# Kernel tuning notes

Hardware: AMD Instinct MI355X
Metric: run time of the kernel (lower is better)

The kernel has to match this reference:

```python
import jax, jax.numpy as jnp
import numpy as np
import math

DEPTH = 2
RATIOS = (0.5, 0.5)
K_PROP = 2  # Gra_inc(2)


def _prop(x, ei, ew, K=K_PROP):
    # GCN-style sym-normalized diffusion with implicit self-loops; Gra_inc(K)
    N = x.shape[0]
    row, col = ei[0], ei[1]
    deg = jax.ops.segment_sum(ew, row, num_segments=N) + 1.0  # +1 self-loop
    dinv = jax.lax.rsqrt(deg)
    norm = dinv[row] * ew * dinv[col]          # [E]
    self_n = (dinv * dinv)[:, None]            # [N,1]
    h, out = x, x
    for _ in range(K):
        h = jax.ops.segment_sum(norm[:, None] * h[col], row, num_segments=N) + self_n * h
        out = out + h
    return out


def _conv(x, ei, ew, W):
    return _prop(x @ W, ei, ew)


def _pool(x, ei, ew, pw, ratio):
    # PyG TopKPooling: score = tanh(x.pw/||pw||), keep top ceil(ratio*N) nodes,
    # gate features by score, relabel surviving edges (dropped edges -> weight 0).
    N = x.shape[0]
    k = int(math.ceil(ratio * N))
    score = jnp.tanh(x @ pw / jnp.linalg.norm(pw))
    val, perm = jax.lax.top_k(score, k)
    x2 = x[perm] * val[:, None]
    nm = jnp.full((N,), -1, jnp.int32).at[perm].set(jnp.arange(k, dtype=jnp.int32))
    r, c = nm[ei[0]], nm[ei[1]]
    kept = (r >= 0) & (c >= 0)
    ei2 = jnp.stack([jnp.where(kept, r, 0), jnp.where(kept, c, 0)])
    ew2 = jnp.where(kept, ew, 0.0)
    return x2, ei2, ew2, perm


def setup_inputs() -> dict:
    key = jax.random.key(0)
    ks = jax.random.split(key, 10)
    N, E, C_in, C_hid, C_out = 50000, 800000, 128, 128, 64
    def w(k, i, o):
        return jax.random.normal(k, (i, o), jnp.float32) / np.sqrt(i)
    return {
        "x": jax.random.normal(ks[0], (N, C_in), jnp.float32),
        "edge_index": jax.random.randint(ks[1], (2, E), 0, N, dtype=jnp.int32),
        "Wd0": w(ks[2], C_in, C_hid),
        "Wd1": w(ks[3], C_hid, C_hid),
        "Wd2": w(ks[4], C_hid, C_hid),
        "pw0": jax.random.normal(ks[5], (C_hid,), jnp.float32) / np.sqrt(C_hid),
        "pw1": jax.random.normal(ks[6], (C_hid,), jnp.float32) / np.sqrt(C_hid),
        "Wu0": w(ks[7], C_hid, C_hid),
        "Wu1": w(ks[8], C_hid, C_hid),
        "Wu2": w(ks[9], 2 * C_hid, C_out),
    }


def reference(x, edge_index, Wd0, Wd1, Wd2, pw0, pw1, Wu0, Wu1, Wu2):
    ei = edge_index
    ew = jnp.ones((ei.shape[1],), x.dtype)
    x = jax.nn.relu(_conv(x, ei, ew, Wd0))
    org = x
    xs, eis, ews, perms = [x], [ei], [ew], []
    for i, (pw, Wd) in enumerate(zip((pw0, pw1), (Wd1, Wd2))):
        x, ei, ew, perm = _pool(x, ei, ew, pw, RATIOS[i])
        x = jax.nn.relu(_conv(x, ei, ew, Wd))
        if i < DEPTH - 1:
            xs.append(x); eis.append(ei); ews.append(ew)
        perms.append(perm)
    for i, Wu in enumerate((Wu0, Wu1)):
        j = DEPTH - 1 - i
        res, ei, ew, perm = xs[j], eis[j], ews[j], perms[j]
        up = jnp.zeros_like(res).at[perm].set(x)
        x = res + up  # sum_res skip fusion
        x = _conv(x, ei, ew, Wu)
        if i < DEPTH - 1:
            x = jax.nn.relu(x)
    x = jnp.concatenate([x, org], axis=1)
    return _conv(x, ei, ew, Wu2)
```

## Files before the change

kernel.cpp:

```cpp
#include <hip/hip_runtime.h>
#include <hip/hip_bf16.h>
#include <stdint.h>

#define DEV __device__ __forceinline__

static constexpr int C_HID = 128;

DEV float4 f4_fma(float a, float4 w, float4 acc) {
  acc.x = fmaf(a, w.x, acc.x); acc.y = fmaf(a, w.y, acc.y);
  acc.z = fmaf(a, w.z, acc.z); acc.w = fmaf(a, w.w, acc.w);
  return acc;
}

DEV unsigned bfpack2(float a, float b) {
  unsigned ua = __float_as_uint(a), ub = __float_as_uint(b);
  ua += 0x7FFF + ((ua >> 16) & 1);
  ub += 0x7FFF + ((ub >> 16) & 1);
  return (ua >> 16) | (ub & 0xFFFF0000u);
}
DEV uint2 bfpack4(float4 v) { return make_uint2(bfpack2(v.x, v.y), bfpack2(v.z, v.w)); }
DEV float4 bfunpack4(uint2 u) {
  return make_float4(__uint_as_float(u.x << 16), __uint_as_float(u.x & 0xFFFF0000u),
                     __uint_as_float(u.y << 16), __uint_as_float(u.y & 0xFFFF0000u));
}

__global__ void scorekeys_kernel(const float* __restrict__ x, const float* __restrict__ pw,
                                 float* __restrict__ score, unsigned long long* __restrict__ keys,
                                 int N) {
  int row = blockIdx.x * 4 + (threadIdx.x >> 6);
  int lane = threadIdx.x & 63;
  if (row >= N) return;
  float p0 = pw[lane], p1 = pw[lane + 64];
  float pn = p0 * p0 + p1 * p1;
  const float* xr = x + (size_t)row * C_HID;
  float s = xr[lane] * p0 + xr[lane + 64] * p1;
#pragma unroll
  for (int o = 32; o > 0; o >>= 1) {
    s += __shfl_xor(s, o, 64);
    pn += __shfl_xor(pn, o, 64);
  }
  if (lane == 0) {
    float sc = tanhf(s / sqrtf(pn));
    score[row] = sc;
    unsigned u = __float_as_uint(sc);
    u ^= (u >> 31) ? 0xFFFFFFFFu : 0x80000000u;
    keys[row] = (((unsigned long long)(~u)) << 16) | (unsigned)row;
  }
}

__global__ void select_hist1_kernel(const unsigned long long* __restrict__ keys, int N,
                                    int* __restrict__ hist) {
  int i = blockIdx.x * 256 + threadIdx.x;
  if (i >= N) return;
  int bin = (int)((keys[i] >> 32) & 0xFFFF);
  atomicAdd(&hist[bin + ((blockIdx.x & 3) << 16)], 1);
}

__global__ void hist_merge_kernel(int* __restrict__ hist) {
  int b = blockIdx.x * 256 + threadIdx.x;
  hist[b] = hist[b] + hist[b + 65536] + hist[b + 2 * 65536] + hist[b + 3 * 65536];
}

__global__ void select_hist_kernel(const unsigned long long* __restrict__ keys, int N,
                                   const unsigned long long* __restrict__ prefix,
                                   int shift, unsigned long long M, int* __restrict__ hist) {
  int i = blockIdx.x * 256 + threadIdx.x;
  if (i >= N) return;
  unsigned long long P = *prefix;
  unsigned long long key = keys[i];
  if (((key ^ P) & M) == 0)
    atomicAdd(&hist[(int)((key >> shift) & 0xFFFF)], 1);
}

__global__ void select_find_kernel(const int* __restrict__ hist,
                                   unsigned long long* __restrict__ prefix,
                                   int* __restrict__ rem, int shift, int* __restrict__ ctr,
                                   int k) {
  int t = threadIdx.x;
  int base = t * 64;
  int s = 0;
#pragma unroll
  for (int j = 0; j < 64; ++j) s += hist[base + j];
  int lane = t & 63, w = t >> 6;
  int v = s;
  for (int o = 1; o < 64; o <<= 1) { int u = __shfl_up(v, o, 64); if (lane >= o) v += u; }
  __shared__ int ws[16];
  if (lane == 63) ws[w] = v;
  __syncthreads();
  if (t < 16) {
    int u = ws[t];
    for (int o = 1; o < 16; o <<= 1) { int uu = __shfl_up(u, o, 64); if (t >= o) u += uu; }
    ws[t] = u;
  }
  __syncthreads();
  int incl = v + (w > 0 ? ws[w - 1] : 0);
  int excl = incl - s;
  int R = (shift == 32) ? k : *rem;
  if (excl < R && incl >= R) {
    int c = excl, b = base;
    for (int j = 0; j < 64; ++j) {
      int h = hist[base + j];
      if (c + h >= R) { b = base + j; break; }
      c += h;
    }
    if (shift == 32) *prefix = ((unsigned long long)b) << shift;
    else             *prefix |= ((unsigned long long)b) << shift;
    *rem = R - c;
    if (shift == 0) *ctr = 0;
  }
}

__global__ void select_enum_kernel(const unsigned long long* __restrict__ keys, int N,
                                   const unsigned long long* __restrict__ Tptr,
                                   int* __restrict__ ctr, int* __restrict__ perm,
                                   int* __restrict__ nm) {
  int i = blockIdx.x * 256 + threadIdx.x;
  if (i >= N) return;
  unsigned long long T = *Tptr;
  if (keys[i] <= T) { int r = atomicAdd(ctr, 1); perm[r] = i; nm[i] = r; }
  else nm[i] = -1;
}

__global__ void pool_gather_kernel(const float* __restrict__ xold, const float* __restrict__ score,
                                   const int* __restrict__ perm, float* __restrict__ xnew, int k) {
  int j = blockIdx.x * 2 + (threadIdx.x >> 7);
  int f = threadIdx.x & 127;
  if (j >= k) return;
  int src = perm[j];
  xnew[(size_t)j * C_HID + f] = xold[(size_t)src * C_HID + f] * score[src];
}

DEV bool map_edge(int a, int b, const int* m0, const int* m1, int& r, int& c) {
  r = a; c = b;
  if (m0) { r = m0[r]; c = m0[c]; if ((r | c) < 0) return false; }
  if (m1) { r = m1[r]; c = m1[c]; if ((r | c) < 0) return false; }
  return true;
}

__global__ void edge_count_kernel(const int* __restrict__ ei, int E, int* __restrict__ cnt) {
  int e = blockIdx.x * 256 + threadIdx.x;
  if (e >= E) return;
  atomicAdd(&cnt[ei[e]], 1);
}

__global__ void edge_fill_kernel(const int* __restrict__ ei, int E,
                                 const int* __restrict__ rowptr, int* __restrict__ fc,
                                 int* __restrict__ colv) {
  int e = blockIdx.x * 256 + threadIdx.x;
  if (e >= E) return;
  int r = ei[e], c = ei[E + e];
  int pos = rowptr[r] + atomicAdd(&fc[r], 1);
  colv[pos] = c;
}

#define CEPT 7
__global__ __launch_bounds__(1024) void edge_count_compact_kernel(
    const int* __restrict__ ei, int E, const int* m0, const int* m1,
    int* __restrict__ cnt, int2* __restrict__ pairs, int* __restrict__ pctr) {
  int tid = threadIdx.x;
  int gbase = blockIdx.x * (1024 * CEPT) + tid;
  int rs[CEPT], cs[CEPT];
  int myn = 0;
#pragma unroll
  for (int i = 0; i < CEPT; ++i) {
    int e = gbase + i * 1024;
    int r, c;
    bool keep = (e < E) && map_edge(ei[e], ei[E + e], m0, m1, r, c);
    rs[i] = keep ? r : -1;
    cs[i] = keep ? c : 0;
    if (keep) { atomicAdd(&cnt[r], 1); ++myn; }
  }
  int lane = tid & 63, w = tid >> 6;
  int v = myn;
  for (int o = 1; o < 64; o <<= 1) { int u = __shfl_up(v, o, 64); if (lane >= o) v += u; }
  __shared__ int ws[16];
  __shared__ int bbase;
  if (lane == 63) ws[w] = v;
  __syncthreads();
  if (tid < 16) {
    int u = ws[tid];
    for (int o = 1; o < 16; o <<= 1) { int uu = __shfl_up(u, o, 64); if (tid >= o) u += uu; }
    ws[tid] = u;
  }
  __syncthreads();
  int excl = v - myn + (w > 0 ? ws[w - 1] : 0);
  if (tid == 1023) bbase = atomicAdd(pctr, excl + myn);
  __syncthreads();
  int pos = bbase + excl;
#pragma unroll
  for (int i = 0; i < CEPT; ++i)
    if (rs[i] >= 0) pairs[pos++] = make_int2(rs[i], cs[i]);
}

__global__ void edge_fill_compact_kernel(const int2* __restrict__ pairs, const int* __restrict__ pctr,
                                         const int* __restrict__ rowptr, int* __restrict__ fc,
                                         int* __restrict__ colv) {
  int i = blockIdx.x * 256 + threadIdx.x;
  if (i >= *pctr) return;
  int2 pr = pairs[i];
  int pos = rowptr[pr.x] + atomicAdd(&fc[pr.x], 1);
  colv[pos] = pr.y;
}

__global__ void scan_partial_kernel(const int* __restrict__ cnt, int n, int* __restrict__ bsum) {
  int i = blockIdx.x * 256 + threadIdx.x;
  int v = (i < n) ? cnt[i] : 0;
#pragma unroll
  for (int o = 32; o > 0; o >>= 1) v += __shfl_down(v, o, 64);
  __shared__ int ws[4];
  if ((threadIdx.x & 63) == 0) ws[threadIdx.x >> 6] = v;
  __syncthreads();
  if (threadIdx.x == 0) bsum[blockIdx.x] = ws[0] + ws[1] + ws[2] + ws[3];
}

__global__ void scan_blocksums_kernel(int* __restrict__ bsum, int nb) {
  int t = threadIdx.x;
  int v = (t < nb) ? bsum[t] : 0;
  int lane = t & 63, w = t >> 6;
  for (int o = 1; o < 64; o <<= 1) { int u = __shfl_up(v, o, 64); if (lane >= o) v += u; }
  __shared__ int ws[16];
  if (lane == 63) ws[w] = v;
  __syncthreads();
  if (t < 16) {
    int u = ws[t];
    for (int o = 1; o < 16; o <<= 1) { int uu = __shfl_up(u, o, 64); if (t >= o) u += uu; }
    ws[t] = u;
  }
  __syncthreads();
  if (t < nb) bsum[t] = v + (w > 0 ? ws[w - 1] : 0);
}

__global__ void scan_scatter_kernel(const int* __restrict__ cnt, int n,
                                    const int* __restrict__ bsum,
                                    int* __restrict__ rowptr, float* __restrict__ dinv,
                                    int* __restrict__ fc) {
  int i = blockIdx.x * 256 + threadIdx.x;
  int v = (i < n) ? cnt[i] : 0;
  int lane = threadIdx.x & 63, w = threadIdx.x >> 6;
  int s = v;
  for (int o = 1; o < 64; o <<= 1) { int u = __shfl_up(s, o, 64); if (lane >= o) s += u; }
  __shared__ int ws[4];
  __shared__ int wo[4];
  if (lane == 63) ws[w] = s;
  __syncthreads();
  if (threadIdx.x == 0) { int c = 0; for (int j = 0; j < 4; ++j) { wo[j] = c; c += ws[j]; } }
  __syncthreads();
  int excl = s - v + wo[w] + (blockIdx.x > 0 ? bsum[blockIdx.x - 1] : 0);
  if (i < n) {
    rowptr[i] = excl;
    dinv[i] = rsqrtf((float)v + 1.0f);
    fc[i] = 0;
    if (i == n - 1) rowptr[n] = excl + v;
  }
}

template <int FIRST, int RELU>
__global__ void spmm_kernel(const int* __restrict__ rowptr, const int* __restrict__ colv,
                            const float* __restrict__ dinv,
                            const float* __restrict__ h_in, const float* __restrict__ x0,
                            float* __restrict__ out, int M, int C) {
  int lanes = C >> 2;
  int rpb = 256 / lanes;
  int r = blockIdx.x * rpb + (int)threadIdx.x / lanes;
  int lane = (int)threadIdx.x % lanes;
  if (r >= M) return;
  float d = dinv[r];
  const float4* hin4 = (const float4*)h_in;
  size_t base = (size_t)r * lanes + lane;
  float4 self = hin4[base];
  float sn = d * d;
  float4 v = make_float4(sn * self.x, sn * self.y, sn * self.z, sn * self.w);
  int e0 = rowptr[r], e1 = rowptr[r + 1];
  int e = e0;
  for (; e + 8 <= e1; e += 8) {
    int cc[8];
#pragma unroll
    for (int i = 0; i < 8; ++i) cc[i] = colv[e + i];
    float4 hh[8];
#pragma unroll
    for (int i = 0; i < 8; ++i) hh[i] = hin4[(size_t)cc[i] * lanes + lane];
    float ww[8];
#pragma unroll
    for (int i = 0; i < 8; ++i) ww[i] = d * dinv[cc[i]];
#pragma unroll
    for (int i = 0; i < 8; ++i) v = f4_fma(ww[i], hh[i], v);
  }
  for (; e < e1; ++e) {
    int c = colv[e];
    float w = d * dinv[c];
    float4 h = hin4[(size_t)c * lanes + lane];
    v = f4_fma(w, h, v);
  }
  if (FIRST) {
    ((float4*)out)[base] = v;
  } else {
    float4 a = ((const float4*)x0)[base];
    a.x += self.x + v.x; a.y += self.y + v.y; a.z += self.z + v.z; a.w += self.w + v.w;
    if (RELU) { a.x = fmaxf(a.x, 0.f); a.y = fmaxf(a.y, 0.f); a.z = fmaxf(a.z, 0.f); a.w = fmaxf(a.w, 0.f); }
    ((float4*)out)[base] = a;
  }
}

template <int FIRST, int RELU>
__global__ void spmm_bf16_kernel(const int* __restrict__ rowptr, const int* __restrict__ colv,
                                 const float* __restrict__ dinv,
                                 const ushort* __restrict__ hb, const float* __restrict__ x0,
                                 void* __restrict__ outp, int M, int C) {
  int lanes = C >> 2;
  int rpb = 256 / lanes;
  int r = blockIdx.x * rpb + (int)threadIdx.x / lanes;
  int lane = (int)threadIdx.x % lanes;
  if (r >= M) return;
  float d = dinv[r];
  const uint2* hb2 = (const uint2*)hb;
  size_t base = (size_t)r * lanes + lane;
  float4 self = bfunpack4(hb2[base]);
  float sn = d * d;
  float4 v = make_float4(sn * self.x, sn * self.y, sn * self.z, sn * self.w);
  int e0 = rowptr[r], e1 = rowptr[r + 1];
  int e = e0;
  for (; e + 8 <= e1; e += 8) {
    int cc[8];
#pragma unroll
    for (int i = 0; i < 8; ++i) cc[i] = colv[e + i];
    uint2 hh[8];
#pragma unroll
    for (int i = 0; i < 8; ++i) hh[i] = hb2[(size_t)cc[i] * lanes + lane];
    float ww[8];
#pragma unroll
    for (int i = 0; i < 8; ++i) ww[i] = d * dinv[cc[i]];
#pragma unroll
    for (int i = 0; i < 8; ++i) v = f4_fma(ww[i], bfunpack4(hh[i]), v);
  }
  for (; e < e1; ++e) {
    int c = colv[e];
    float w = d * dinv[c];
    v = f4_fma(w, bfunpack4(hb2[(size_t)c * lanes + lane]), v);
  }
  if (FIRST) {
    ((uint2*)outp)[base] = bfpack4(v);
  } else {
    float4 a = ((const float4*)x0)[base];
    a.x += self.x + v.x; a.y += self.y + v.y; a.z += self.z + v.z; a.w += self.w + v.w;
    if (RELU) { a.x = fmaxf(a.x, 0.f); a.y = fmaxf(a.y, 0.f); a.z = fmaxf(a.z, 0.f); a.w = fmaxf(a.w, 0.f); }
    ((float4*)outp)[base] = a;
  }
}

template <int NC, int KT, int SKIP, int ADDIN, int MIRROR>
__global__ __launch_bounds__(256) void gemm_kernel(const float* __restrict__ A1, int K1,
                                                   const float* __restrict__ W,
                                                   float* __restrict__ Cd, int M,
                                                   const float* __restrict__ up,
                                                   const int* __restrict__ nm,
                                                   const float* __restrict__ addv,
                                                   ushort* __restrict__ bh) {
  constexpr int KTILE = 32;
  constexpr int AP = KTILE + 4;
  constexpr int CG = NC / 4;
  constexpr int RG = 256 / CG;
  constexpr int RPT = 64 / RG;
  __shared__ float Wl[KTILE * NC];
  __shared__ float Al[64 * AP];
  int tid = threadIdx.x;
  int r0 = blockIdx.x * 64;
  int cg = tid % CG, rg = tid / CG;
  float4 acc[RPT];
#pragma unroll
  for (int m = 0; m < RPT; ++m) acc[m] = make_float4(0.f, 0.f, 0.f, 0.f);

  for (int k0 = 0; k0 < KT; k0 += KTILE) {
    const float4* Wg = (const float4*)(W + (size_t)k0 * NC);
    for (int idx = tid; idx < KTILE * NC / 4; idx += 256)
      ((float4*)Wl)[idx] = Wg[idx];
#pragma unroll
    for (int s = 0; s < (64 * KTILE / 4) / 256; ++s) {
      int f4i = tid + s * 256;
      int row = f4i >> 3;
      int kk = (f4i & 7) << 2;
      int gr = r0 + row, gk = k0 + kk;
      float4 v = make_float4(0.f, 0.f, 0.f, 0.f);
      if (gr < M) {
        v = *(const float4*)(A1 + (size_t)gr * K1 + gk);
        if (SKIP) {
          int j = nm[gr];
          if (j >= 0) {
            float4 u = *(const float4*)(up + (size_t)j * K1 + gk);
            v.x += u.x; v.y += u.y; v.z += u.z; v.w += u.w;
          }
        }
      }
      *(float4*)&Al[row * AP + kk] = v;
    }
    __syncthreads();
#pragma unroll
    for (int kk0 = 0; kk0 < KTILE; kk0 += 4) {
      float4 a4[RPT];
#pragma unroll
      for (int m = 0; m < RPT; ++m)
        a4[m] = *(const float4*)&Al[(rg * RPT + m) * AP + kk0];
#pragma unroll
      for (int j = 0; j < 4; ++j) {
        float4 w = *(const float4*)&Wl[(kk0 + j) * NC + cg * 4];
#pragma unroll
        for (int m = 0; m < RPT; ++m) {
          float a = (j == 0) ? a4[m].x : (j == 1) ? a4[m].y : (j == 2) ? a4[m].z : a4[m].w;
          acc[m] = f4_fma(a, w, acc[m]);
        }
      }
    }
    __syncthreads();
  }
#pragma unroll
  for (int m = 0; m < RPT; ++m) {
    int gr = r0 + rg * RPT + m;
    if (gr < M) {
      float4 o = acc[m];
      if (ADDIN) {
        float4 u = *(const float4*)(addv + (size_t)gr * NC + cg * 4);
        o.x += u.x; o.y += u.y; o.z += u.z; o.w += u.w;
      }
      *(float4*)(Cd + (size_t)gr * NC + cg * 4) = o;
      if (MIRROR) ((uint2*)bh)[(size_t)gr * CG + cg] = bfpack4(o);
    }
  }
}

extern "C" void kernel_launch(void* const* d_in, const int* in_sizes, int n_in,
                              void* d_out, int out_size, void* d_ws, size_t ws_size,
                              hipStream_t stream) {
  const float* x   = (const float*)d_in[0];
  const int*   ei  = (const int*)d_in[1];
  const float* Wd0 = (const float*)d_in[2];
  const float* Wd1 = (const float*)d_in[3];
  const float* Wd2 = (const float*)d_in[4];
  const float* pw0 = (const float*)d_in[5];
  const float* pw1 = (const float*)d_in[6];
  const float* Wu0 = (const float*)d_in[7];
  const float* Wu1 = (const float*)d_in[8];
  const float* Wu2 = (const float*)d_in[9];
  float* out = (float*)d_out;

  const int C = C_HID;
  int N0 = in_sizes[0] / C;
  int E  = in_sizes[1] / 2;
  int k1 = (N0 + 1) / 2;
  int k2 = (k1 + 1) / 2;

  char* p = (char*)d_ws;
  auto alloc = [&](size_t bytes) { char* q = p; p += (bytes + 255) & ~(size_t)255; return q; };
  float* org   = (float*)alloc((size_t)N0 * C * 4);
  float* b0    = (float*)alloc((size_t)N0 * C * 4);
  float* b1    = (float*)alloc((size_t)N0 * C * 4);
  float* b2    = (float*)alloc((size_t)N0 * C * 4);
  float* x1res = (float*)alloc((size_t)k1 * C * 4);
  ushort* bh   = (ushort*)alloc((size_t)N0 * C * 2);
  ushort* h1h  = (ushort*)alloc((size_t)N0 * C * 2);
  float* score = (float*)alloc((size_t)N0 * 4);
  unsigned long long* keys = (unsigned long long*)alloc((size_t)N0 * 8);
  int* perm0 = (int*)alloc((size_t)k1 * 4);
  int* perm1 = (int*)alloc((size_t)k2 * 4);
  int* map0  = (int*)alloc((size_t)N0 * 4);
  int* map1  = (int*)alloc((size_t)k1 * 4);
  int* cnt   = (int*)alloc((size_t)N0 * 4);
  int* fc    = (int*)alloc((size_t)N0 * 4);
  int* rp0   = (int*)alloc((size_t)(N0 + 1) * 4);
  int* rp1   = (int*)alloc((size_t)(k1 + 1) * 4);
  int* rp2   = (int*)alloc((size_t)(k2 + 1) * 4);
  float* dinv0 = (float*)alloc((size_t)N0 * 4);
  float* dinv1 = (float*)alloc((size_t)k1 * 4);
  float* dinv2 = (float*)alloc((size_t)k2 * 4);
  int* col0 = (int*)alloc((size_t)E * 4);
  int* col1 = (int*)alloc((size_t)E * 4);
  int* col2 = (int*)alloc((size_t)E * 4);
  int2* pairs = (int2*)alloc((size_t)E * 8);
  int* hist12 = (int*)alloc((size_t)12 * 65536 * 4);
  int* bsum = (int*)alloc(1024 * 4);
  float* Wcat1 = (float*)alloc((size_t)128 * 64 * 4);
  unsigned long long* selT = (unsigned long long*)alloc(64);
  int* selRem = (int*)alloc(64);
  int* selCtr = (int*)alloc(64);
  int* pctr = (int*)alloc(64);

  dim3 b256(256);
  int egrid = (E + 255) / 256;
  int cgrid = (E + 1024 * CEPT - 1) / (1024 * CEPT);
  int g0_128 = (N0 + 7) / 8;
  int g1_128 = (k1 + 7) / 8;
  int g2_128 = (k2 + 7) / 8;
  int g0_64  = (N0 + 15) / 16;

  auto scan_csr = [&](int n, int* rowptr, float* dinv) {
    int g = (n + 255) / 256;
    scan_partial_kernel<<<g, b256, 0, stream>>>(cnt, n, bsum);
    scan_blocksums_kernel<<<1, 1024, 0, stream>>>(bsum, g);
    scan_scatter_kernel<<<g, b256, 0, stream>>>(cnt, n, bsum, rowptr, dinv, fc);
  };

  auto topk_select = [&](int N, int k, int* perm, int* nm, int* histb) {
    int g = (N + 255) / 256;
    select_hist1_kernel<<<g, b256, 0, stream>>>(keys, N, histb);
    hist_merge_kernel<<<256, b256, 0, stream>>>(histb);
    select_find_kernel<<<1, 1024, 0, stream>>>(histb, selT, selRem, 32, selCtr, k);
    select_hist_kernel<<<g, b256, 0, stream>>>(keys, N, selT, 16, ~0ull << 32, histb + 4 * 65536);
    select_find_kernel<<<1, 1024, 0, stream>>>(histb + 4 * 65536, selT, selRem, 16, selCtr, k);
    select_hist_kernel<<<g, b256, 0, stream>>>(keys, N, selT, 0, ~0ull << 16, histb + 5 * 65536);
    select_find_kernel<<<1, 1024, 0, stream>>>(histb + 5 * 65536, selT, selRem, 0, selCtr, k);
    select_enum_kernel<<<g, b256, 0, stream>>>(keys, N, selT, selCtr, perm, nm);
  };

  hipMemsetAsync(hist12, 0, (size_t)12 * 65536 * 4, stream);

  gemm_kernel<64, 128, 0, 0, 0><<<2, b256, 0, stream>>>(Wu1, 128, Wu2, Wcat1, 128, nullptr, nullptr, nullptr, nullptr);

  hipMemsetAsync(cnt, 0, (size_t)N0 * 4, stream);
  edge_count_kernel<<<egrid, b256, 0, stream>>>(ei, E, cnt);
  scan_csr(N0, rp0, dinv0);
  edge_fill_kernel<<<egrid, b256, 0, stream>>>(ei, E, rp0, fc, col0);

  gemm_kernel<128, 128, 0, 0, 0><<<(N0 + 63) / 64, b256, 0, stream>>>(x, 128, Wd0, b0, N0, nullptr, nullptr, nullptr, nullptr);
  spmm_kernel<1, 0><<<g0_128, b256, 0, stream>>>(rp0, col0, dinv0, b0, nullptr, b1, N0, 128);
  spmm_kernel<0, 1><<<g0_128, b256, 0, stream>>>(rp0, col0, dinv0, b1, b0, org, N0, 128);

  scorekeys_kernel<<<(N0 + 3) / 4, b256, 0, stream>>>(org, pw0, score, keys, N0);
  topk_select(N0, k1, perm0, map0, hist12);
  pool_gather_kernel<<<(k1 + 1) / 2, b256, 0, stream>>>(org, score, perm0, b0, k1);

  hipMemsetAsync(cnt, 0, (size_t)k1 * 4, stream);
  hipMemsetAsync(pctr, 0, 4, stream);
  edge_count_compact_kernel<<<cgrid, 1024, 0, stream>>>(ei, E, map0, nullptr, cnt, pairs, pctr);
  scan_csr(k1, rp1, dinv1);
  edge_fill_compact_kernel<<<egrid, b256, 0, stream>>>(pairs, pctr, rp1, fc, col1);

  gemm_kernel<128, 128, 0, 0, 0><<<(k1 + 63) / 64, b256, 0, stream>>>(b0, 128, Wd1, b1, k1, nullptr, nullptr, nullptr, nullptr);
  spmm_kernel<1, 0><<<g1_128, b256, 0, stream>>>(rp1, col1, dinv1, b1, nullptr, b2, k1, 128);
  spmm_kernel<0, 1><<<g1_128, b256, 0, stream>>>(rp1, col1, dinv1, b2, b1, x1res, k1, 128);

  scorekeys_kernel<<<(k1 + 3) / 4, b256, 0, stream>>>(x1res, pw1, score, keys, k1);
  topk_select(k1, k2, perm1, map1, hist12 + 6 * 65536);
  pool_gather_kernel<<<(k2 + 1) / 2, b256, 0, stream>>>(x1res, score, perm1, b0, k2);

  hipMemsetAsync(cnt, 0, (size_t)k2 * 4, stream);
  hipMemsetAsync(pctr, 0, 4, stream);
  edge_count_compact_kernel<<<cgrid, 1024, 0, stream>>>(ei, E, map0, map1, cnt, pairs, pctr);
  scan_csr(k2, rp2, dinv2);
  edge_fill_compact_kernel<<<egrid, b256, 0, stream>>>(pairs, pctr, rp2, fc, col2);

  gemm_kernel<128, 128, 0, 0, 1><<<(k2 + 63) / 64, b256, 0, stream>>>(b0, 128, Wd2, b1, k2, nullptr, nullptr, nullptr, bh);
  spmm_bf16_kernel<1, 0><<<g2_128, b256, 0, stream>>>(rp2, col2, dinv2, bh, nullptr, h1h, k2, 128);
  spmm_bf16_kernel<0, 1><<<g2_128, b256, 0, stream>>>(rp2, col2, dinv2, h1h, b1, b0, k2, 128);

  gemm_kernel<128, 128, 1, 0, 1><<<(k1 + 63) / 64, b256, 0, stream>>>(x1res, 128, Wu0, b1, k1, b0, map1, nullptr, bh);
  spmm_bf16_kernel<1, 0><<<g1_128, b256, 0, stream>>>(rp1, col1, dinv1, bh, nullptr, h1h, k1, 128);
  spmm_bf16_kernel<0, 1><<<g1_128, b256, 0, stream>>>(rp1, col1, dinv1, h1h, b1, b0, k1, 128);

  gemm_kernel<64, 128, 1, 0, 1><<<(N0 + 63) / 64, b256, 0, stream>>>(org, 128, Wcat1, b2, N0, b0, map0, nullptr, bh);
  spmm_bf16_kernel<1, 0><<<g0_64, b256, 0, stream>>>(rp0, col0, dinv0, bh, nullptr, h1h, N0, 64);
  spmm_bf16_kernel<0, 0><<<g0_64, b256, 0, stream>>>(rp0, col0, dinv0, h1h, b2, b2, N0, 64);
  gemm_kernel<64, 128, 0, 1, 1><<<(N0 + 63) / 64, b256, 0, stream>>>(org, 128, Wu2 + (size_t)128 * 64, b0, N0, nullptr, nullptr, b2, bh);
  spmm_bf16_kernel<1, 0><<<g0_64, b256, 0, stream>>>(rp0, col0, dinv0, bh, nullptr, h1h, N0, 64);
  spmm_bf16_kernel<0, 0><<<g0_64, b256, 0, stream>>>(rp0, col0, dinv0, h1h, b0, out, N0, 64);
}
```

Measured before the change: 766.6 us.

## Fuse top-k selection and CSR build into persistent cooperative kernels

Replaces the chain of small top-k radix-select kernels and the count/scan/fill CSR kernels with two cooperative kernels that use grid-wide syncs between phases, removing many launches and memsets. The top-k find step now uses a two-level group sum read by one block, and enumeration uses block-level scan with one atomic per block. Grid syncs over 512 blocks add their own cost, and the grid-stride loops change parallelism and atomic contention compared with one-thread-per-element launches.

```diff
diff --git a/kernel.cpp b/kernel.cpp
--- a/kernel.cpp
+++ b/kernel.cpp
@@ -1,6 +1,9 @@
 #include <hip/hip_runtime.h>
 #include <hip/hip_bf16.h>
+#include <hip/hip_cooperative_groups.h>
 #include <stdint.h>
+
+namespace cg = cooperative_groups;
 
 #define DEV __device__ __forceinline__
 
@@ -48,77 +51,105 @@
   }
 }
 
-__global__ void select_hist1_kernel(const unsigned long long* __restrict__ keys, int N,
-                                    int* __restrict__ hist) {
-  int i = blockIdx.x * 256 + threadIdx.x;
-  if (i >= N) return;
-  int bin = (int)((keys[i] >> 32) & 0xFFFF);
-  atomicAdd(&hist[bin + ((blockIdx.x & 3) << 16)], 1);
-}
-
-__global__ void hist_merge_kernel(int* __restrict__ hist) {
-  int b = blockIdx.x * 256 + threadIdx.x;
-  hist[b] = hist[b] + hist[b + 65536] + hist[b + 2 * 65536] + hist[b + 3 * 65536];
-}
-
-__global__ void select_hist_kernel(const unsigned long long* __restrict__ keys, int N,
-                                   const unsigned long long* __restrict__ prefix,
-                                   int shift, unsigned long long M, int* __restrict__ hist) {
-  int i = blockIdx.x * 256 + threadIdx.x;
-  if (i >= N) return;
-  unsigned long long P = *prefix;
-  unsigned long long key = keys[i];
-  if (((key ^ P) & M) == 0)
-    atomicAdd(&hist[(int)((key >> shift) & 0xFFFF)], 1);
-}
-
-__global__ void select_find_kernel(const int* __restrict__ hist,
-                                   unsigned long long* __restrict__ prefix,
-                                   int* __restrict__ rem, int shift, int* __restrict__ ctr,
-                                   int k) {
-  int t = threadIdx.x;
-  int base = t * 64;
-  int s = 0;
-#pragma unroll
-  for (int j = 0; j < 64; ++j) s += hist[base + j];
-  int lane = t & 63, w = t >> 6;
-  int v = s;
-  for (int o = 1; o < 64; o <<= 1) { int u = __shfl_up(v, o, 64); if (lane >= o) v += u; }
-  __shared__ int ws[16];
-  if (lane == 63) ws[w] = v;
-  __syncthreads();
-  if (t < 16) {
-    int u = ws[t];
-    for (int o = 1; o < 16; o <<= 1) { int uu = __shfl_up(u, o, 64); if (t >= o) u += uu; }
-    ws[t] = u;
-  }
-  __syncthreads();
-  int incl = v + (w > 0 ? ws[w - 1] : 0);
-  int excl = incl - s;
-  int R = (shift == 32) ? k : *rem;
-  if (excl < R && incl >= R) {
-    int c = excl, b = base;
-    for (int j = 0; j < 64; ++j) {
-      int h = hist[base + j];
-      if (c + h >= R) { b = base + j; break; }
-      c += h;
-    }
-    if (shift == 32) *prefix = ((unsigned long long)b) << shift;
-    else             *prefix |= ((unsigned long long)b) << shift;
-    *rem = R - c;
-    if (shift == 0) *ctr = 0;
-  }
-}
-
-__global__ void select_enum_kernel(const unsigned long long* __restrict__ keys, int N,
-                                   const unsigned long long* __restrict__ Tptr,
-                                   int* __restrict__ ctr, int* __restrict__ perm,
-                                   int* __restrict__ nm) {
-  int i = blockIdx.x * 256 + threadIdx.x;
-  if (i >= N) return;
-  unsigned long long T = *Tptr;
-  if (keys[i] <= T) { int r = atomicAdd(ctr, 1); perm[r] = i; nm[i] = r; }
-  else nm[i] = -1;
+__global__ void topk_kernel(const unsigned long long* __restrict__ keys, int N, int k,
+                            int* __restrict__ hist, int* __restrict__ gsum,
+                            unsigned long long* __restrict__ prefixp, int* __restrict__ remp,
+                            int* __restrict__ ctr, int* __restrict__ perm,
+                            int* __restrict__ nm) {
+  cg::grid_group grid = cg::this_grid();
+  int gtid = blockIdx.x * blockDim.x + threadIdx.x;
+  int nthreads = gridDim.x * blockDim.x;
+
+  for (int i = gtid; i < 6 * 65536; i += nthreads) hist[i] = 0;
+  if (gtid == 0) *ctr = 0;
+  grid.sync();
+
+  for (int i = gtid; i < N; i += nthreads)
+    atomicAdd(&hist[(int)((keys[i] >> 32) & 0xFFFF) + ((blockIdx.x & 3) << 16)], 1);
+  grid.sync();
+  for (int b = gtid; b < 65536; b += nthreads)
+    hist[b] += hist[b + 65536] + hist[b + 2 * 65536] + hist[b + 3 * 65536];
+  grid.sync();
+
+  for (int pass = 0; pass < 3; ++pass) {
+    int shift = 32 - 16 * pass;
+    int* h = (pass == 0) ? hist : hist + (3 + pass) * 65536;
+    if (pass > 0) {
+      unsigned long long M = (pass == 1) ? (~0ull << 32) : (~0ull << 16);
+      unsigned long long P = *prefixp;
+      for (int i = gtid; i < N; i += nthreads) {
+        unsigned long long key = keys[i];
+        if (((key ^ P) & M) == 0)
+          atomicAdd(&h[(int)((key >> shift) & 0xFFFF)], 1);
+      }
+      grid.sync();
+    }
+    if (gtid < 1024) {
+      int s = 0, base = gtid * 64;
+      for (int j = 0; j < 64; ++j) s += h[base + j];
+      gsum[gtid] = s;
+    }
+    grid.sync();
+    if (blockIdx.x == 0) {
+      int t = threadIdx.x;
+      int s = gsum[4 * t] + gsum[4 * t + 1] + gsum[4 * t + 2] + gsum[4 * t + 3];
+      int lane = t & 63, w = t >> 6;
+      int v = s;
+      for (int o = 1; o < 64; o <<= 1) { int u = __shfl_up(v, o, 64); if (lane >= o) v += u; }
+      __shared__ int ws[4];
+      __shared__ int wo[4];
+      if (lane == 63) ws[w] = v;
+      __syncthreads();
+      if (t == 0) { int c = 0; for (int j = 0; j < 4; ++j) { wo[j] = c; c += ws[j]; } }
+      __syncthreads();
+      int incl = v + wo[w];
+      int excl = incl - s;
+      int R = (pass == 0) ? k : *remp;
+      if (excl < R && incl >= R) {
+        int c = excl, bfound = -1;
+        for (int g = 4 * t; g < 4 * t + 4 && bfound < 0; ++g) {
+          if (c + gsum[g] >= R) {
+            int base = g * 64;
+            for (int j = 0; j < 64; ++j) {
+              int hv = h[base + j];
+              if (c + hv >= R) { bfound = base + j; break; }
+              c += hv;
+            }
+          } else c += gsum[g];
+        }
+        if (pass == 0) *prefixp = ((unsigned long long)bfound) << shift;
+        else           *prefixp |= ((unsigned long long)bfound) << shift;
+        *remp = R - c;
+      }
+      __syncthreads();
+    }
+    grid.sync();
+  }
+
+  unsigned long long T = *prefixp;
+  for (int base = blockIdx.x * 256; base < N; base += nthreads) {
+    int i = base + threadIdx.x;
+    bool keep = (i < N) && (keys[i] <= T);
+    int lane = threadIdx.x & 63, w = threadIdx.x >> 6;
+    int sc = keep ? 1 : 0;
+    for (int o = 1; o < 64; o <<= 1) { int u = __shfl_up(sc, o, 64); if (lane >= o) sc += u; }
+    __shared__ int bws[4];
+    __shared__ int bbase;
+    if (lane == 63) bws[w] = sc;
+    __syncthreads();
+    if (threadIdx.x == 0) {
+      int tot = bws[0] + bws[1] + bws[2] + bws[3];
+      bbase = atomicAdd(ctr, tot);
+      int c = 0;
+      for (int j = 0; j < 4; ++j) { int tmp = bws[j]; bws[j] = c; c += tmp; }
+    }
+    __syncthreads();
+    if (i < N) {
+      if (keep) { int r = bbase + bws[w] + sc - 1; perm[r] = i; nm[i] = r; }
+      else nm[i] = -1;
+    }
+    __syncthreads();
+  }
 }
 
 __global__ void pool_gather_kernel(const float* __restrict__ xold, const float* __restrict__ score,
@@ -137,120 +168,112 @@
   return true;
 }
 
-__global__ void edge_count_kernel(const int* __restrict__ ei, int E, int* __restrict__ cnt) {
-  int e = blockIdx.x * 256 + threadIdx.x;
-  if (e >= E) return;
-  atomicAdd(&cnt[ei[e]], 1);
-}
-
-__global__ void edge_fill_kernel(const int* __restrict__ ei, int E,
-                                 const int* __restrict__ rowptr, int* __restrict__ fc,
-                                 int* __restrict__ colv) {
-  int e = blockIdx.x * 256 + threadIdx.x;
-  if (e >= E) return;
-  int r = ei[e], c = ei[E + e];
-  int pos = rowptr[r] + atomicAdd(&fc[r], 1);
-  colv[pos] = c;
-}
-
-#define CEPT 7
-__global__ __launch_bounds__(1024) void edge_count_compact_kernel(
-    const int* __restrict__ ei, int E, const int* m0, const int* m1,
-    int* __restrict__ cnt, int2* __restrict__ pairs, int* __restrict__ pctr) {
-  int tid = threadIdx.x;
-  int gbase = blockIdx.x * (1024 * CEPT) + tid;
-  int rs[CEPT], cs[CEPT];
-  int myn = 0;
-#pragma unroll
-  for (int i = 0; i < CEPT; ++i) {
-    int e = gbase + i * 1024;
-    int r, c;
-    bool keep = (e < E) && map_edge(ei[e], ei[E + e], m0, m1, r, c);
-    rs[i] = keep ? r : -1;
-    cs[i] = keep ? c : 0;
-    if (keep) { atomicAdd(&cnt[r], 1); ++myn; }
-  }
-  int lane = tid & 63, w = tid >> 6;
-  int v = myn;
-  for (int o = 1; o < 64; o <<= 1) { int u = __shfl_up(v, o, 64); if (lane >= o) v += u; }
-  __shared__ int ws[16];
-  __shared__ int bbase;
-  if (lane == 63) ws[w] = v;
-  __syncthreads();
-  if (tid < 16) {
-    int u = ws[tid];
-    for (int o = 1; o < 16; o <<= 1) { int uu = __shfl_up(u, o, 64); if (tid >= o) u += uu; }
-    ws[tid] = u;
-  }
-  __syncthreads();
-  int excl = v - myn + (w > 0 ? ws[w - 1] : 0);
-  if (tid == 1023) bbase = atomicAdd(pctr, excl + myn);
-  __syncthreads();
-  int pos = bbase + excl;
-#pragma unroll
-  for (int i = 0; i < CEPT; ++i)
-    if (rs[i] >= 0) pairs[pos++] = make_int2(rs[i], cs[i]);
-}
-
-__global__ void edge_fill_compact_kernel(const int2* __restrict__ pairs, const int* __restrict__ pctr,
-                                         const int* __restrict__ rowptr, int* __restrict__ fc,
-                                         int* __restrict__ colv) {
-  int i = blockIdx.x * 256 + threadIdx.x;
-  if (i >= *pctr) return;
-  int2 pr = pairs[i];
-  int pos = rowptr[pr.x] + atomicAdd(&fc[pr.x], 1);
-  colv[pos] = pr.y;
-}
-
-__global__ void scan_partial_kernel(const int* __restrict__ cnt, int n, int* __restrict__ bsum) {
-  int i = blockIdx.x * 256 + threadIdx.x;
-  int v = (i < n) ? cnt[i] : 0;
-#pragma unroll
-  for (int o = 32; o > 0; o >>= 1) v += __shfl_down(v, o, 64);
-  __shared__ int ws[4];
-  if ((threadIdx.x & 63) == 0) ws[threadIdx.x >> 6] = v;
-  __syncthreads();
-  if (threadIdx.x == 0) bsum[blockIdx.x] = ws[0] + ws[1] + ws[2] + ws[3];
-}
-
-__global__ void scan_blocksums_kernel(int* __restrict__ bsum, int nb) {
-  int t = threadIdx.x;
-  int v = (t < nb) ? bsum[t] : 0;
-  int lane = t & 63, w = t >> 6;
-  for (int o = 1; o < 64; o <<= 1) { int u = __shfl_up(v, o, 64); if (lane >= o) v += u; }
-  __shared__ int ws[16];
-  if (lane == 63) ws[w] = v;
-  __syncthreads();
-  if (t < 16) {
-    int u = ws[t];
-    for (int o = 1; o < 16; o <<= 1) { int uu = __shfl_up(u, o, 64); if (t >= o) u += uu; }
-    ws[t] = u;
-  }
-  __syncthreads();
-  if (t < nb) bsum[t] = v + (w > 0 ? ws[w - 1] : 0);
-}
-
-__global__ void scan_scatter_kernel(const int* __restrict__ cnt, int n,
-                                    const int* __restrict__ bsum,
-                                    int* __restrict__ rowptr, float* __restrict__ dinv,
-                                    int* __restrict__ fc) {
-  int i = blockIdx.x * 256 + threadIdx.x;
-  int v = (i < n) ? cnt[i] : 0;
-  int lane = threadIdx.x & 63, w = threadIdx.x >> 6;
-  int s = v;
-  for (int o = 1; o < 64; o <<= 1) { int u = __shfl_up(s, o, 64); if (lane >= o) s += u; }
-  __shared__ int ws[4];
-  __shared__ int wo[4];
-  if (lane == 63) ws[w] = s;
-  __syncthreads();
-  if (threadIdx.x == 0) { int c = 0; for (int j = 0; j < 4; ++j) { wo[j] = c; c += ws[j]; } }
-  __syncthreads();
-  int excl = s - v + wo[w] + (blockIdx.x > 0 ? bsum[blockIdx.x - 1] : 0);
-  if (i < n) {
-    rowptr[i] = excl;
-    dinv[i] = rsqrtf((float)v + 1.0f);
-    fc[i] = 0;
-    if (i == n - 1) rowptr[n] = excl + v;
+template <int MAPPED>
+__global__ void csr_build_kernel(const int* __restrict__ ei, int E,
+                                 const int* m0, const int* m1, int n,
+                                 int* __restrict__ cnt, int* __restrict__ rowptr,
+                                 float* __restrict__ dinv, int* __restrict__ fc,
+                                 int* __restrict__ colv, int2* __restrict__ pairs,
+                                 int* __restrict__ pctr, int* __restrict__ bsum) {
+  cg::grid_group grid = cg::this_grid();
+  int gtid = blockIdx.x * blockDim.x + threadIdx.x;
+  int nthreads = gridDim.x * blockDim.x;
+
+  for (int i = gtid; i < n; i += nthreads) cnt[i] = 0;
+  if (MAPPED && gtid == 0) *pctr = 0;
+  grid.sync();
+
+  if (MAPPED) {
+    for (int base = blockIdx.x * 256; base < E; base += nthreads) {
+      int e = base + threadIdx.x;
+      int r = 0, c = 0;
+      bool keep = (e < E) && map_edge(ei[e], ei[E + e], m0, m1, r, c);
+      if (keep) atomicAdd(&cnt[r], 1);
+      int lane = threadIdx.x & 63, w = threadIdx.x >> 6;
+      int sc = keep ? 1 : 0;
+      for (int o = 1; o < 64; o <<= 1) { int u = __shfl_up(sc, o, 64); if (lane >= o) sc += u; }
+      __shared__ int bws[4];
+      __shared__ int bb;
+      if (lane == 63) bws[w] = sc;
+      __syncthreads();
+      if (threadIdx.x == 0) {
+        int tot = bws[0] + bws[1] + bws[2] + bws[3];
+        bb = atomicAdd(pctr, tot);
+        int cc = 0;
+        for (int j = 0; j < 4; ++j) { int t = bws[j]; bws[j] = cc; cc += t; }
+      }
+      __syncthreads();
+      if (keep) pairs[bb + bws[w] + sc - 1] = make_int2(r, c);
+      __syncthreads();
+    }
+  } else {
+    for (int e = gtid; e < E; e += nthreads) atomicAdd(&cnt[ei[e]], 1);
+  }
+  grid.sync();
+
+  int nch = (n + 255) / 256;
+  for (int cidx = blockIdx.x; cidx < nch; cidx += gridDim.x) {
+    int i = cidx * 256 + threadIdx.x;
+    int v = (i < n) ? cnt[i] : 0;
+#pragma unroll
+    for (int o = 32; o > 0; o >>= 1) v += __shfl_down(v, o, 64);
+    __shared__ int rws[4];
+    if ((threadIdx.x & 63) == 0) rws[threadIdx.x >> 6] = v;
+    __syncthreads();
+    if (threadIdx.x == 0) bsum[cidx] = rws[0] + rws[1] + rws[2] + rws[3];
+    __syncthreads();
+  }
+  grid.sync();
+  if (blockIdx.x == 0) {
+    int t = threadIdx.x;
+    int v = (t < nch) ? bsum[t] : 0;
+    int lane = t & 63, w = t >> 6;
+    for (int o = 1; o < 64; o <<= 1) { int u = __shfl_up(v, o, 64); if (lane >= o) v += u; }
+    __shared__ int sws[4];
+    __shared__ int swo[4];
+    if (lane == 63) sws[w] = v;
+    __syncthreads();
+    if (t == 0) { int c = 0; for (int j = 0; j < 4; ++j) { swo[j] = c; c += sws[j]; } }
+    __syncthreads();
+    if (t < nch) bsum[t] = v + swo[w];
+  }
+  grid.sync();
+  for (int cidx = blockIdx.x; cidx < nch; cidx += gridDim.x) {
+    int i = cidx * 256 + threadIdx.x;
+    int v = (i < n) ? cnt[i] : 0;
+    int lane = threadIdx.x & 63, w = threadIdx.x >> 6;
+    int s = v;
+    for (int o = 1; o < 64; o <<= 1) { int u = __shfl_up(s, o, 64); if (lane >= o) s += u; }
+    __shared__ int sws2[4];
+    __shared__ int swo2[4];
+    if (lane == 63) sws2[w] = s;
+    __syncthreads();
+    if (threadIdx.x == 0) { int c = 0; for (int j = 0; j < 4; ++j) { int t2 = sws2[j]; swo2[j] = c; c += t2; } }
+    __syncthreads();
+    int excl = s - v + swo2[w] + (cidx > 0 ? bsum[cidx - 1] : 0);
+    if (i < n) {
+      rowptr[i] = excl;
+      dinv[i] = rsqrtf((float)v + 1.0f);
+      fc[i] = 0;
+      if (i == n - 1) rowptr[n] = excl + v;
+    }
+    __syncthreads();
+  }
+  grid.sync();
+
+  if (MAPPED) {
+    int np = *pctr;
+    for (int i = gtid; i < np; i += nthreads) {
+      int2 pr = pairs[i];
+      int pos = rowptr[pr.x] + atomicAdd(&fc[pr.x], 1);
+      colv[pos] = pr.y;
+    }
+  } else {
+    for (int e = gtid; e < E; e += nthreads) {
+      int r = ei[e], c = ei[E + e];
+      int pos = rowptr[r] + atomicAdd(&fc[r], 1);
+      colv[pos] = c;
+    }
   }
 }
 
@@ -474,7 +497,8 @@
   int* col1 = (int*)alloc((size_t)E * 4);
   int* col2 = (int*)alloc((size_t)E * 4);
   int2* pairs = (int2*)alloc((size_t)E * 8);
-  int* hist12 = (int*)alloc((size_t)12 * 65536 * 4);
+  int* hist = (int*)alloc((size_t)6 * 65536 * 4);
+  int* gsum = (int*)alloc(1024 * 4);
   int* bsum = (int*)alloc(1024 * 4);
   float* Wcat1 = (float*)alloc((size_t)128 * 64 * 4);
   unsigned long long* selT = (unsigned long long*)alloc(64);
@@ -483,68 +507,52 @@
   int* pctr = (int*)alloc(64);
 
   dim3 b256(256);
-  int egrid = (E + 255) / 256;
-  int cgrid = (E + 1024 * CEPT - 1) / (1024 * CEPT);
+  dim3 coopGrid(512), coopBlk(256);
   int g0_128 = (N0 + 7) / 8;
   int g1_128 = (k1 + 7) / 8;
   int g2_128 = (k2 + 7) / 8;
   int g0_64  = (N0 + 15) / 16;
 
-  auto scan_csr = [&](int n, int* rowptr, float* dinv) {
-    int g = (n + 255) / 256;
-    scan_partial_kernel<<<g, b256, 0, stream>>>(cnt, n, bsum);
-    scan_blocksums_kernel<<<1, 1024, 0, stream>>>(bsum, g);
-    scan_scatter_kernel<<<g, b256, 0, stream>>>(cnt, n, bsum, rowptr, dinv, fc);
+  auto csr_build = [&](int mapped, const int* m0, const int* m1, int n,
+                       int* rowptr, float* dinv, int* colv) {
+    const int* m0_ = m0; const int* m1_ = m1; int n_ = n; int E_ = E;
+    void* args[] = { (void*)&ei, (void*)&E_, (void*)&m0_, (void*)&m1_, (void*)&n_,
+                     (void*)&cnt, (void*)&rowptr, (void*)&dinv, (void*)&fc, (void*)&colv,
+                     (void*)&pairs, (void*)&pctr, (void*)&bsum };
+    hipLaunchCooperativeKernel(mapped ? (void*)csr_build_kernel<1> : (void*)csr_build_kernel<0>,
+                               coopGrid, coopBlk, args, 0, stream);
   };
 
-  auto topk_select = [&](int N, int k, int* perm, int* nm, int* histb) {
-    int g = (N + 255) / 256;
-    select_hist1_kernel<<<g, b256, 0, stream>>>(keys, N, histb);
-    hist_merge_kernel<<<256, b256, 0, stream>>>(histb);
-    select_find_kernel<<<1, 1024, 0, stream>>>(histb, selT, selRem, 32, selCtr, k);
-    select_hist_kernel<<<g, b256, 0, stream>>>(keys, N, selT, 16, ~0ull << 32, histb + 4 * 65536);
-    select_find_kernel<<<1, 1024, 0, stream>>>(histb + 4 * 65536, selT, selRem, 16, selCtr, k);
-    select_hist_kernel<<<g, b256, 0, stream>>>(keys, N, selT, 0, ~0ull << 16, histb + 5 * 65536);
-    select_find_kernel<<<1, 1024, 0, stream>>>(histb + 5 * 65536, selT, selRem, 0, selCtr, k);
-    select_enum_kernel<<<g, b256, 0, stream>>>(keys, N, selT, selCtr, perm, nm);
+  auto topk_select = [&](int N, int k, int* perm, int* nm) {
+    int N_ = N; int k_ = k; int* perm_ = perm; int* nm_ = nm;
+    void* args[] = { (void*)&keys, (void*)&N_, (void*)&k_, (void*)&hist, (void*)&gsum,
+                     (void*)&selT, (void*)&selRem, (void*)&selCtr, (void*)&perm_, (void*)&nm_ };
+    hipLaunchCooperativeKernel((void*)topk_kernel, coopGrid, coopBlk, args, 0, stream);
   };
 
-  hipMemsetAsync(hist12, 0, (size_t)12 * 65536 * 4, stream);
-
   gemm_kernel<64, 128, 0, 0, 0><<<2, b256, 0, stream>>>(Wu1, 128, Wu2, Wcat1, 128, nullptr, nullptr, nullptr, nullptr);
 
-  hipMemsetAsync(cnt, 0, (size_t)N0 * 4, stream);
-  edge_count_kernel<<<egrid, b256, 0, stream>>>(ei, E, cnt);
-  scan_csr(N0, rp0, dinv0);
-  edge_fill_kernel<<<egrid, b256, 0, stream>>>(ei, E, rp0, fc, col0);
+  csr_build(0, nullptr, nullptr, N0, rp0, dinv0, col0);
 
   gemm_kernel<128, 128, 0, 0, 0><<<(N0 + 63) / 64, b256, 0, stream>>>(x, 128, Wd0, b0, N0, nullptr, nullptr, nullptr, nullptr);
   spmm_kernel<1, 0><<<g0_128, b256, 0, stream>>>(rp0, col0, dinv0, b0, nullptr, b1, N0, 128);
   spmm_kernel<0, 1><<<g0_128, b256, 0, stream>>>(rp0, col0, dinv0, b1, b0, org, N0, 128);
 
   scorekeys_kernel<<<(N0 + 3) / 4, b256, 0, stream>>>(org, pw0, score, keys, N0);
-  topk_select(N0, k1, perm0, map0, hist12);
+  topk_select(N0, k1, perm0, map0);
   pool_gather_kernel<<<(k1 + 1) / 2, b256, 0, stream>>>(org, score, perm0, b0, k1);
 
-  hipMemsetAsync(cnt, 0, (size_t)k1 * 4, stream);
-  hipMemsetAsync(pctr, 0, 4, stream);
-  edge_count_compact_kernel<<<cgrid, 1024, 0, stream>>>(ei, E, map0, nullptr, cnt, pairs, pctr);
-  scan_csr(k1, rp1, dinv1);
-  edge_fill_compact_kernel<<<egrid, b256, 0, stream>>>(pairs, pctr, rp1, fc, col1);
+  csr_build(1, map0, nullptr, k1, rp1, dinv1, col1);
 
   gemm_kernel<128, 128, 0, 0, 0><<<(k1 + 63) / 64, b256, 0, stream>>>(b0, 128, Wd1, b1, k1, nullptr, nullptr, nullptr, nullptr);
   spmm_kernel<1, 0><<<g1_128, b256, 0, stream>>>(rp1, col1, dinv1, b1, nullptr, b2, k1, 128);
   spmm_kernel<0, 1><<<g1_128, b256, 0, stream>>>(rp1, col1, dinv1, b2, b1, x1res, k1, 128);
 
   scorekeys_kernel<<<(k1 + 3) / 4, b256, 0, stream>>>(x1res, pw1, score, keys, k1);
-  topk_select(k1, k2, perm1, map1, hist12 + 6 * 65536);
+  topk_select(k1, k2, perm1, map1);
   pool_gather_kernel<<<(k2 + 1) / 2, b256, 0, stream>>>(x1res, score, perm1, b0, k2);
 
-  hipMemsetAsync(cnt, 0, (size_t)k2 * 4, stream);
-  hipMemsetAsync(pctr, 0, 4, stream);
-  edge_count_compact_kernel<<<cgrid, 1024, 0, stream>>>(ei, E, map0, map1, cnt, pairs, pctr);
-  scan_csr(k2, rp2, dinv2);
-  edge_fill_compact_kernel<<<egrid, b256, 0, stream>>>(pairs, pctr, rp2, fc, col2);
+  csr_build(1, map0, map1, k2, rp2, dinv2, col2);
 
   gemm_kernel<128, 128, 0, 0, 1><<<(k2 + 63) / 64, b256, 0, stream>>>(b0, 128, Wd2, b1, k2, nullptr, nullptr, nullptr, bh);
   spmm_bf16_kernel<1, 0><<<g2_128, b256, 0, stream>>>(rp2, col2, dinv2, bh, nullptr, h1h, k2, 128);
```

Result: slower. 2.640 ms (+244.4%).
